# Kernel optimization log

Measured on AMD Instinct MI355X. Metric: run time of the kernel, lower is better.

The kernel has to match this reference:

```python
import jax, jax.numpy as jnp
import numpy as np

B, N, C = 4, 4096, 16
HID, OUT = 64, 64
ALL_K, K = 128, 32          # k + k_pos = 32
KD, KDP = 8, 6              # k_dilated, k_dilated_pos
EPS = 1e-5
NEG_SLOPE = 0.2


def setup_inputs() -> dict:
    ks = jax.random.split(jax.random.key(0), 12)
    C2, C4 = 2 * C, 4 * C
    return {
        "x": jax.random.normal(ks[0], (B, N, C), jnp.float32),
        "pos": jax.random.normal(ks[1], (B, N, 3), jnp.float32),
        "W1": jax.random.normal(ks[2], (C2, C2), jnp.float32) * 0.1,
        "g1": jnp.ones((C2,), jnp.float32),
        "b1": jnp.zeros((C2,), jnp.float32),
        "W2": jax.random.normal(ks[3], (HID, C4), jnp.float32) * 0.05,
        "g2": jnp.ones((HID,), jnp.float32),
        "b2": jnp.zeros((HID,), jnp.float32),
        "W3": jax.random.normal(ks[4], (OUT, HID), jnp.float32) * 0.05,
        "g3": jnp.ones((OUT,), jnp.float32),
        "b3": jnp.zeros((OUT,), jnp.float32),
    }


def pdist2(a):
    # squared pairwise distances (same top-k ordering as cdist p=2, and
    # avoids sqrt(0) on the diagonal). a: (B,N,D) -> (B,N,N)
    sq = jnp.sum(a * a, axis=-1)
    d = sq[:, :, None] + sq[:, None, :] - 2.0 * jnp.einsum('bnd,bmd->bnm', a, a)
    return jnp.maximum(d, 0.0)


def knn_excl_self(d2, k):
    # k nearest excluding self (self is the unique 0-distance nearest point)
    idx = jax.lax.top_k(-d2, k + 1)[1]
    return idx[..., 1:]


def fps(pts, npoint):
    # pts: (M, Kn, 3). Deterministic start at index 0 (torch version uses a
    # random start; only the sampled index set differs, math is identical).
    M, Kn, _ = pts.shape
    rows = jnp.arange(M)

    def body(i, state):
        centroids, distance, farthest = state
        centroids = centroids.at[:, i].set(farthest)
        centroid = pts[rows, farthest][:, None, :]            # (M,1,3)
        dist = jnp.sum((pts - centroid) ** 2, axis=-1)         # (M,Kn)
        distance = jnp.minimum(distance, dist)
        farthest = jnp.argmax(distance, axis=-1).astype(jnp.int32)
        return centroids, distance, farthest

    init = (jnp.zeros((M, npoint), jnp.int32),
            jnp.full((M, Kn), 1e10, jnp.float32),
            jnp.zeros((M,), jnp.int32))
    centroids, _, _ = jax.lax.fori_loop(0, npoint, body, init)
    return centroids


def edge_feat(feat, idx):
    # feat: (B,N,D) node features, idx: (B,N,Kn) neighbor indices
    # returns cat(neighbor - center, center): (B,N,Kn,2D)  (edge_function 249)
    nbr = feat[jnp.arange(feat.shape[0])[:, None, None], idx]  # (B,N,Kn,D)
    ctr = feat[:, :, None, :]
    return jnp.concatenate([nbr - ctr, jnp.broadcast_to(ctr, nbr.shape)], axis=-1)


def bn_lrelu(h, g, b):
    # BatchNorm2d with track_running_stats=False -> always batch stats.
    # h: (B,N,Kn,Cc), stats over (B,N,Kn) per channel.
    mu = jnp.mean(h, axis=(0, 1, 2), keepdims=True)
    var = jnp.var(h, axis=(0, 1, 2), keepdims=True)
    h = (h - mu) * jax.lax.rsqrt(var + EPS) * g + b
    return jnp.where(h > 0, h, NEG_SLOPE * h)


def reference(x, pos, W1, g1, b1, W2, g2, b2, W3, g3, b3):
    # --- dilated neighborhood: all_k nearest by position, FPS down to k ---
    cd2 = pdist2(pos)                                   # (B,N,N)
    idx_l = jax.lax.top_k(-cd2, ALL_K)[1]               # (B,N,ALL_K) incl. self
    idx_l_flat = idx_l.reshape(B * N, ALL_K)
    pts = pos.reshape(B * N, 3)[idx_l_flat]             # (B*N, ALL_K, 3)
    idx_fps_local = fps(pts, K)                         # (B*N, K)
    idx_fps = jnp.take_along_axis(idx_l_flat, idx_fps_local, axis=1)
    idx_fps = idx_fps.reshape(B, N, K)                  # (B,N,K)

    # --- dual kNN graph: k_dilated by feature distance + k_dilated_pos by pos ---
    idx_feat = knn_excl_self(pdist2(x), KD)             # (B,N,KD)
    idx_pos = knn_excl_self(cd2, KDP)                   # (B,N,KDP)
    idx1 = jnp.concatenate([idx_feat, idx_pos], axis=2)  # (B,N,KD+KDP)

    # --- conv1x1-BN-LeakyReLU on dual-graph edge features, max over nbrs ---
    e1 = edge_feat(x, idx1)                             # (B,N,14,2C)
    h1 = bn_lrelu(jnp.einsum('bnkc,oc->bnko', e1, W1), g1, b1)
    f1 = jnp.max(h1, axis=2)                            # (B,N,2C)

    # --- edge features on FPS-dilated graph, two conv1x1-BN-LeakyReLU ---
    e2 = edge_feat(f1, idx_fps)                         # (B,N,K,4C)
    h2 = bn_lrelu(jnp.einsum('bnkc,hc->bnkh', e2, W2), g2, b2)
    h3 = bn_lrelu(jnp.einsum('bnkh,oh->bnko', h2, W3), g3, b3)
    out = jnp.max(h3, axis=2)                           # (B,N,OUT)
    return out, idx1
```

## Files before the change

kernel.cpp:

```cpp
#include <hip/hip_runtime.h>

#define NPTS 4096
#define BNROWS 16384

__device__ __forceinline__ float lrelu(float h) { return h > 0.f ? h : 0.2f * h; }

#define WSYNC asm volatile("s_waitcnt lgkmcnt(0)" ::: "memory")

__global__ __launch_bounds__(512) void knn_pos_kernel(
    const float* __restrict__ pos, int* __restrict__ idx_l,
    int* __restrict__ idx1_i, float* __restrict__ idx1_f)
{
  __shared__ unsigned long long cKey[8][512];
  __shared__ unsigned int cCnt[8];
  int tid = threadIdx.x;
  int w = tid >> 6, lane = tid & 63;
  int r = blockIdx.x * 8 + w;
  int b = r >> 12, n = r & 4095;
  const float* pb = pos + (size_t)b * NPTS * 3;
  float cx = pb[n*3+0], cy = pb[n*3+1], cz = pb[n*3+2];
  if (lane == 0) cCnt[w] = 0u;
  WSYNC;

  unsigned int qp[32];
  int m1 = 65536, m2 = 65536, m3 = 65536;
  #pragma unroll
  for (int t = 0; t < 32; ++t) {
    unsigned int wq = 0u;
    #pragma unroll
    for (int h = 0; h < 2; ++h) {
      int j = (2*t + h) * 64 + lane;
      float dx = cx - pb[j*3+0], dy = cy - pb[j*3+1], dz = cz - pb[j*3+2];
      float d2 = dx*dx + dy*dy + dz*dz;
      int q = (int)(d2 * 1000.0f);
      q = q < 0 ? 0 : (q > 65535 ? 65535 : q);
      wq |= ((unsigned int)q) << (16*h);
      int nm1 = min(m1, q);
      int nm2 = min(m2, max(m1, q));
      int nm3 = min(m3, max(m2, q));
      m1 = nm1; m2 = nm2; m3 = nm3;
    }
    qp[t] = wq;
  }
  int lo = 0, hi = 65535;
  #pragma unroll
  for (int it = 0; it < 16; ++it) {
    int mid = (lo + hi) >> 1;
    int cnt = __popcll(__ballot(m3 <= mid));
    if (cnt >= 43) hi = mid; else lo = mid + 1;
  }
  unsigned int qt = (unsigned int)lo + 2u;

  #pragma unroll
  for (int t = 0; t < 32; ++t) {
    unsigned int wq = qp[t];
    unsigned int q0 = wq & 0xffffu, q1 = wq >> 16;
    if (q0 <= qt) { unsigned int p = atomicAdd(&cCnt[w], 1u); if (p < 512u) cKey[w][p] = (unsigned long long)((2*t)*64 + lane); }
    if (q1 <= qt) { unsigned int p = atomicAdd(&cCnt[w], 1u); if (p < 512u) cKey[w][p] = (unsigned long long)((2*t+1)*64 + lane); }
  }
  WSYNC;
  unsigned int nc = cCnt[w]; if (nc > 512u) nc = 512u;
  int M = (nc <= 256u) ? 256 : 512;
  int EPL = M >> 6;

  double cxd = (double)cx, cyd = (double)cy, czd = (double)cz;
  for (int t = 0; t < EPL; ++t) {
    int c = lane + (t << 6);
    unsigned long long kk = ~0ull;
    if (c < (int)nc) {
      int id = (int)cKey[w][c];
      double dx = cxd - (double)pb[id*3+0];
      double dy = cyd - (double)pb[id*3+1];
      double dz = czd - (double)pb[id*3+2];
      double d2 = dx*dx + dy*dy + dz*dz;
      unsigned long long bits = (unsigned long long)__double_as_longlong(d2);
      kk = (bits & ~0xFFFull) | (unsigned long long)(unsigned int)id;
    }
    cKey[w][c] = kk;
  }
  WSYNC;

  for (int k = 2; k <= M; k <<= 1) {
    for (int j = k >> 1; j > 0; j >>= 1) {
      for (int t = 0; t < EPL; ++t) {
        int i = lane + (t << 6);
        int ixj = i ^ j;
        if (ixj > i) {
          unsigned long long ka = cKey[w][i], kb = cKey[w][ixj];
          bool up = ((i & k) == 0);
          if ((ka > kb) == up) { cKey[w][i] = kb; cKey[w][ixj] = ka; }
        }
      }
      WSYNC;
    }
  }
  idx_l[(size_t)r * 128 + lane]      = (int)(cKey[w][lane] & 0xFFFull);
  idx_l[(size_t)r * 128 + lane + 64] = (int)(cKey[w][lane + 64] & 0xFFFull);
  if (lane < 6) {
    int v = (int)(cKey[w][1 + lane] & 0xFFFull);
    idx1_i[r * 14 + 8 + lane] = v;
    idx1_f[r * 14 + 8 + lane] = (float)v;
  }
}

__global__ __launch_bounds__(512) void knn_feat_kernel(
    const float* __restrict__ x, int* __restrict__ idx1_i, float* __restrict__ idx1_f)
{
  __shared__ float ctrf[8][16];
  __shared__ float4 cm2[8][5];
  __shared__ unsigned short lmin[8][512];
  __shared__ int cand[8][192];
  __shared__ unsigned int cCnt[8];
  __shared__ unsigned short qtS[8];
  int tid = threadIdx.x;
  int rbase = blockIdx.x * 8;
  int b = rbase >> 12;
  const float* xb = x + (size_t)b * NPTS * 16;

  if (tid < 128) {
    int rr = tid >> 4, c = tid & 15;
    float v = xb[(size_t)((rbase + rr) & 4095) * 16 + c];
    ctrf[rr][c] = v;
    ((float*)&cm2[rr][0])[c] = -2.0f * v;
  }
  if (tid < 8) cCnt[tid] = 0u;
  __syncthreads();
  if (tid < 8) {
    float s = 0.f;
    for (int c = 0; c < 16; ++c) { float v = ctrf[tid][c]; s += v * v; }
    cm2[tid][4].x = s;
  }
  __syncthreads();

  unsigned int qp[8][4];
  int minq[8];
  #pragma unroll
  for (int r = 0; r < 8; ++r) minq[r] = 65536;

  #pragma unroll
  for (int pp = 0; pp < 4; ++pp) {
    int j0 = tid + 512 * (2*pp);
    int j1 = j0 + 512;
    const float4* xj0 = (const float4*)(xb + (size_t)j0 * 16);
    const float4* xj1 = (const float4*)(xb + (size_t)j1 * 16);
    float4 a0 = xj0[0], a1 = xj0[1], a2 = xj0[2], a3 = xj0[3];
    float4 b0 = xj1[0], b1 = xj1[1], b2 = xj1[2], b3 = xj1[3];
    float va[16] = {a0.x,a0.y,a0.z,a0.w, a1.x,a1.y,a1.z,a1.w,
                    a2.x,a2.y,a2.z,a2.w, a3.x,a3.y,a3.z,a3.w};
    float vb[16] = {b0.x,b0.y,b0.z,b0.w, b1.x,b1.y,b1.z,b1.w,
                    b2.x,b2.y,b2.z,b2.w, b3.x,b3.y,b3.z,b3.w};
    float pna = 0.f, pnb = 0.f;
    #pragma unroll
    for (int c = 0; c < 16; ++c) { pna = fmaf(va[c], va[c], pna); pnb = fmaf(vb[c], vb[c], pnb); }
    #pragma unroll
    for (int r = 0; r < 8; ++r) {
      float4 m0 = cm2[r][0], m1 = cm2[r][1], m2 = cm2[r][2], m3 = cm2[r][3];
      float c2 = cm2[r][4].x;
      float wm[16] = {m0.x,m0.y,m0.z,m0.w, m1.x,m1.y,m1.z,m1.w,
                      m2.x,m2.y,m2.z,m2.w, m3.x,m3.y,m3.z,m3.w};
      float aa = pna + c2, ab = pnb + c2;
      #pragma unroll
      for (int c = 0; c < 16; ++c) { aa = fmaf(wm[c], va[c], aa); ab = fmaf(wm[c], vb[c], ab); }
      int qa = (int)(aa * 400.0f); qa = qa < 0 ? 0 : (qa > 65535 ? 65535 : qa);
      int qb = (int)(ab * 400.0f); qb = qb < 0 ? 0 : (qb > 65535 ? 65535 : qb);
      qp[r][pp] = (unsigned int)qa | ((unsigned int)qb << 16);
      minq[r] = min(minq[r], min(qa, qb));
    }
  }
  #pragma unroll
  for (int r = 0; r < 8; ++r) lmin[r][tid] = (unsigned short)minq[r];
  __syncthreads();

  int w = tid >> 6, lane = tid & 63;
  {
    unsigned short lv[8];
    #pragma unroll
    for (int t = 0; t < 8; ++t) lv[t] = lmin[w][lane + 64*t];
    int lo = 0, hi = 65535;
    #pragma unroll
    for (int it = 0; it < 16; ++it) {
      int mid = (lo + hi) >> 1;
      int cnt = 0;
      #pragma unroll
      for (int t = 0; t < 8; ++t) cnt += __popcll(__ballot((int)lv[t] <= mid));
      if (cnt >= 10) hi = mid; else lo = mid + 1;
    }
    if (lane == 0) qtS[w] = (unsigned short)min(lo + 2, 65535);
  }
  __syncthreads();

  {
    unsigned int qts[8];
    #pragma unroll
    for (int r = 0; r < 8; ++r) qts[r] = qtS[r];
    #pragma unroll
    for (int r = 0; r < 8; ++r) {
      #pragma unroll
      for (int pp = 0; pp < 4; ++pp) {
        unsigned int wq = qp[r][pp];
        unsigned int q0 = wq & 0xffffu, q1 = wq >> 16;
        if (q0 <= qts[r]) { unsigned int p = atomicAdd(&cCnt[r], 1u); if (p < 192u) cand[r][p] = tid + 512*(2*pp); }
        if (q1 <= qts[r]) { unsigned int p = atomicAdd(&cCnt[r], 1u); if (p < 192u) cand[r][p] = tid + 512*(2*pp+1); }
      }
    }
  }
  __syncthreads();

  {
    int nc = (int)cCnt[w]; if (nc > 192) nc = 192;
    double key[3]; int kid[3];
    #pragma unroll
    for (int s = 0; s < 3; ++s) {
      int c = lane + 64*s;
      if (c < nc) {
        int id = cand[w][c];
        const float4* xp = (const float4*)(xb + (size_t)id * 16);
        float4 q0 = xp[0], q1 = xp[1], q2 = xp[2], q3 = xp[3];
        float xv[16] = {q0.x,q0.y,q0.z,q0.w, q1.x,q1.y,q1.z,q1.w,
                        q2.x,q2.y,q2.z,q2.w, q3.x,q3.y,q3.z,q3.w};
        double acc = 0.0;
        #pragma unroll
        for (int c2 = 0; c2 < 16; ++c2) { double d = (double)ctrf[w][c2] - (double)xv[c2]; acc += d * d; }
        key[s] = acc; kid[s] = id;
      } else { key[s] = 1e300; kid[s] = 0x7fffffff; }
    }
    int row = rbase + w;
    for (int it = 0; it < 9; ++it) {
      double bk = key[0]; int bi = kid[0], bs = 0;
      if (key[1] < bk || (key[1] == bk && kid[1] < bi)) { bk = key[1]; bi = kid[1]; bs = 1; }
      if (key[2] < bk || (key[2] == bk && kid[2] < bi)) { bk = key[2]; bi = kid[2]; bs = 2; }
      double rk = bk; int ri = bi;
      #pragma unroll
      for (int off = 32; off > 0; off >>= 1) {
        double ok = __shfl_xor(rk, off, 64);
        int oi = __shfl_xor(ri, off, 64);
        if (ok < rk || (ok == rk && oi < ri)) { rk = ok; ri = oi; }
      }
      if (it > 0 && lane == 0) {
        idx1_i[row * 14 + it - 1] = ri;
        idx1_f[row * 14 + it - 1] = (float)ri;
      }
      if (bi == ri) key[bs] = 1e300;
    }
  }
}

__global__ __launch_bounds__(256) void fps_kernel(
    const float* __restrict__ pos, const int* __restrict__ idx_l, int* __restrict__ idx_fps)
{
  int wave = threadIdx.x >> 6, lane = threadIdx.x & 63;
  int r = blockIdx.x * 4 + wave;
  const int* il = idx_l + (size_t)r * 128;
  int gi0 = il[lane], gi1 = il[lane + 64];
  double x0 = (double)pos[gi0*3+0], y0 = (double)pos[gi0*3+1], z0 = (double)pos[gi0*3+2];
  double x1 = (double)pos[gi1*3+0], y1 = (double)pos[gi1*3+1], z1 = (double)pos[gi1*3+2];
  double d0 = 1e10, d1 = 1e10;
  int far = 0;
  int* outp = idx_fps + (size_t)r * 32;
  for (int i = 0; i < 32; ++i) {
    int ownerLane = far & 63;
    int sel = far >> 6;
    int gsel = sel ? gi1 : gi0;
    int gout = __shfl(gsel, ownerLane, 64);
    if (lane == 0) outp[i] = gout;
    double cx = __shfl(sel ? x1 : x0, ownerLane, 64);
    double cy = __shfl(sel ? y1 : y0, ownerLane, 64);
    double cz = __shfl(sel ? z1 : z0, ownerLane, 64);
    double t0 = (x0-cx)*(x0-cx) + (y0-cy)*(y0-cy) + (z0-cz)*(z0-cz);
    double t1 = (x1-cx)*(x1-cx) + (y1-cy)*(y1-cy) + (z1-cz)*(z1-cz);
    d0 = fmin(d0, t0); d1 = fmin(d1, t1);
    double v; int p;
    if (d1 > d0) { v = d1; p = lane + 64; } else { v = d0; p = lane; }
    for (int off = 32; off > 0; off >>= 1) {
      double ov = __shfl_xor(v, off, 64);
      int op = __shfl_xor(p, off, 64);
      if (ov > v || (ov == v && op < p)) { v = ov; p = op; }
    }
    far = p;
  }
}

__global__ __launch_bounds__(256) void sv_kernel(
    const float* __restrict__ x, const float* __restrict__ W1,
    float* __restrict__ s, float* __restrict__ v)
{
  __shared__ float xs[8][16];
  __shared__ float w1t[512], w1dt[512];
  int tid = threadIdx.x;
  int rbase = blockIdx.x * 8;
  for (int i = tid; i < 512; i += 256) {
    int c = i >> 5, o = i & 31;
    float a = W1[o * 32 + c], bb = W1[o * 32 + 16 + c];
    w1t[i] = a; w1dt[i] = bb - a;
  }
  if (tid < 128) { int rr = tid >> 4, c = tid & 15; xs[rr][c] = x[(size_t)(rbase + rr) * 16 + c]; }
  __syncthreads();
  int rr = tid >> 5, o = tid & 31;
  float sa = 0.f, va = 0.f;
  #pragma unroll
  for (int c = 0; c < 16; ++c) {
    float xv = xs[rr][c];
    sa = fmaf(xv, w1t[c * 32 + o], sa);
    va = fmaf(xv, w1dt[c * 32 + o], va);
  }
  int r = rbase + rr;
  s[(size_t)r * 32 + o] = sa;
  v[(size_t)r * 32 + o] = va;
}

__global__ __launch_bounds__(256) void h1stats_kernel(
    const float* __restrict__ s, const float* __restrict__ v, const int* __restrict__ idx1_i,
    double* __restrict__ slotsH1, float* __restrict__ h1max)
{
  __shared__ int sidx[8][14];
  __shared__ float sred[256], sred2[256];
  int tid = threadIdx.x;
  int rr = tid >> 5, o = tid & 31;
  int rbase = blockIdx.x * 8;
  if (tid < 112) { int q = tid / 14, k = tid % 14; sidx[q][k] = idx1_i[(rbase + q) * 14 + k]; }
  __syncthreads();
  int r = rbase + rr;
  int broff = r & ~4095;
  float vv = v[(size_t)r * 32 + o];
  float m = -3.4e38f, ls = 0.f, lss = 0.f;
  #pragma unroll
  for (int k = 0; k < 14; ++k) {
    int j = sidx[rr][k];
    float val = s[(size_t)(broff + j) * 32 + o] + vv;
    m = fmaxf(m, val);
    ls += val; lss += val * val;
  }
  h1max[(size_t)r * 32 + o] = m;
  sred[tid] = ls; sred2[tid] = lss;
  __syncthreads();
  if (tid < 32) {
    float s2 = 0.f, ss = 0.f;
    #pragma unroll
    for (int j = 0; j < 8; ++j) { s2 += sred[j * 32 + tid]; ss += sred2[j * 32 + tid]; }
    int slot = blockIdx.x & 255;
    atomicAdd(&slotsH1[slot * 64 + tid], (double)s2);
    atomicAdd(&slotsH1[slot * 64 + 32 + tid], (double)ss);
  }
}

__global__ void finalize_stats_kernel(const double* __restrict__ slots, int C, double cnt,
    const float* __restrict__ g, const float* __restrict__ bta, float* __restrict__ scsh)
{
  int o = threadIdx.x;
  if (o < C) {
    double s = 0.0, ss = 0.0;
    for (int slot = 0; slot < 256; ++slot) { s += slots[slot * 2 * C + o]; ss += slots[slot * 2 * C + C + o]; }
    double mu = s / cnt;
    double var = ss / cnt - mu * mu;
    double rs = 1.0 / sqrt(var + 1e-5);
    float sc = (float)rs * g[o];
    float sh = bta[o] - (float)mu * sc;
    scsh[o] = sc;
    scsh[C + o] = sh;
  }
}

__global__ __launch_bounds__(256) void tu_kernel(
    const float* __restrict__ h1max, const float* __restrict__ scsh1, const float* __restrict__ W2,
    float* __restrict__ t, float* __restrict__ u)
{
  __shared__ float f1s[4][32];
  __shared__ float w2t[2048], w2dt[2048];
  int tid = threadIdx.x;
  int rbase = blockIdx.x * 4;
  for (int i = tid; i < 2048; i += 256) {
    int c = i >> 6, o = i & 63;
    float a = W2[o * 64 + c], bb = W2[o * 64 + 32 + c];
    w2t[i] = a; w2dt[i] = bb - a;
  }
  if (tid < 128) {
    int rr = tid >> 5, c = tid & 31;
    f1s[rr][c] = lrelu(h1max[(size_t)(rbase + rr) * 32 + c] * scsh1[c] + scsh1[32 + c]);
  }
  __syncthreads();
  int rr = tid >> 6, o = tid & 63;
  float ta = 0.f, ua = 0.f;
  #pragma unroll
  for (int c = 0; c < 32; ++c) {
    float fv = f1s[rr][c];
    ta = fmaf(fv, w2t[c * 64 + o], ta);
    ua = fmaf(fv, w2dt[c * 64 + o], ua);
  }
  int r = rbase + rr;
  t[(size_t)r * 64 + o] = ta;
  u[(size_t)r * 64 + o] = ua;
}

__global__ __launch_bounds__(256) void h2stats_kernel(
    const float* __restrict__ t, const float* __restrict__ u, const int* __restrict__ idx_fps,
    double* __restrict__ slotsH2)
{
  __shared__ int nids[8][32];
  __shared__ float sred[256], sred2[256];
  int tid = threadIdx.x;
  int o = tid & 63, wv = tid >> 6;
  int rbase = blockIdx.x * 8;
  { int q = tid >> 5, k = tid & 31; nids[q][k] = idx_fps[(rbase + q) * 32 + k]; }
  __syncthreads();
  float ls = 0.f, lss = 0.f;
  for (int rr = 0; rr < 8; ++rr) {
    int r = rbase + rr;
    int broff = r & ~4095;
    float uo = u[(size_t)r * 64 + o];
    #pragma unroll
    for (int i = 0; i < 8; ++i) {
      int k = wv + 4 * i;
      float val = t[(size_t)(broff + nids[rr][k]) * 64 + o] + uo;
      ls += val; lss += val * val;
    }
  }
  sred[tid] = ls; sred2[tid] = lss;
  __syncthreads();
  if (tid < 64) {
    float s2 = sred[tid] + sred[tid + 64] + sred[tid + 128] + sred[tid + 192];
    float ss = sred2[tid] + sred2[tid + 64] + sred2[tid + 128] + sred2[tid + 192];
    int slot = blockIdx.x & 255;
    atomicAdd(&slotsH2[slot * 128 + tid], (double)s2);
    atomicAdd(&slotsH2[slot * 128 + 64 + tid], (double)ss);
  }
}

#define ROWS3 8
__global__ __launch_bounds__(256, 4) void h3_kernel(
    const float* __restrict__ t, const float* __restrict__ u, const int* __restrict__ idx_fps,
    const float* __restrict__ W3, const float* __restrict__ scsh2,
    double* __restrict__ slotsH3, float* __restrict__ h3max)
{
  __shared__ float h2lds[2048];
  __shared__ float wmax[256];
  __shared__ float sred[256], sred2[256];
  __shared__ int nids[ROWS3][32];
  int tid = threadIdx.x;
  int o = tid & 63, wv = tid >> 6;
  float4 w3r[16];
  const float4* w3p = (const float4*)(W3 + o * 64);
  #pragma unroll
  for (int j = 0; j < 16; ++j) w3r[j] = w3p[j];
  float sc2o = scsh2[o], sh2o = scsh2[64 + o];
  int rbase = blockIdx.x * ROWS3;
  { int q = tid >> 5, k = tid & 31; nids[q][k] = idx_fps[(rbase + q) * 32 + k]; }
  float ls = 0.f, lss = 0.f;
  __syncthreads();
  for (int rr = 0; rr < ROWS3; ++rr) {
    int r = rbase + rr;
    int broff = r & ~4095;
    float uo = u[(size_t)r * 64 + o];
    #pragma unroll
    for (int i = 0; i < 8; ++i) {
      int k = wv + 4 * i;
      float val = t[(size_t)(broff + nids[rr][k]) * 64 + o] + uo;
      h2lds[k * 64 + o] = lrelu(val * sc2o + sh2o);
    }
    __syncthreads();
    float kmax = -3.4e38f;
    #pragma unroll
    for (int i = 0; i < 8; ++i) {
      int k = wv + 4 * i;
      const float4* hp = (const float4*)(h2lds + k * 64);
      float acc = 0.f;
      #pragma unroll
      for (int j = 0; j < 16; ++j) {
        float4 h = hp[j];
        acc = fmaf(h.x, w3r[j].x, acc); acc = fmaf(h.y, w3r[j].y, acc);
        acc = fmaf(h.z, w3r[j].z, acc); acc = fmaf(h.w, w3r[j].w, acc);
      }
      ls += acc; lss += acc * acc;
      kmax = fmaxf(kmax, acc);
    }
    wmax[tid] = kmax;
    __syncthreads();
    if (tid < 64) {
      float m = fmaxf(fmaxf(wmax[tid], wmax[64 + tid]), fmaxf(wmax[128 + tid], wmax[192 + tid]));
      h3max[(size_t)r * 64 + tid] = m;
    }
  }
  sred[tid] = ls; sred2[tid] = lss;
  __syncthreads();
  if (tid < 64) {
    float s2 = sred[tid] + sred[tid + 64] + sred[tid + 128] + sred[tid + 192];
    float ss = sred2[tid] + sred2[tid + 64] + sred2[tid + 128] + sred2[tid + 192];
    int slot = blockIdx.x & 255;
    atomicAdd(&slotsH3[slot * 128 + tid], (double)s2);
    atomicAdd(&slotsH3[slot * 128 + 64 + tid], (double)ss);
  }
}

__global__ void out_kernel(const float* __restrict__ h3max, const float* __restrict__ scsh3,
                           float* __restrict__ out)
{
  int i = blockIdx.x * 256 + threadIdx.x;
  int o = i & 63;
  out[i] = lrelu(h3max[i] * scsh3[o] + scsh3[64 + o]);
}

extern "C" void kernel_launch(void* const* d_in, const int* in_sizes, int n_in,
                              void* d_out, int out_size, void* d_ws, size_t ws_size,
                              hipStream_t stream) {
  (void)in_sizes; (void)n_in; (void)out_size; (void)ws_size;
  const float* x   = (const float*)d_in[0];
  const float* pos = (const float*)d_in[1];
  const float* W1  = (const float*)d_in[2];
  const float* g1  = (const float*)d_in[3];
  const float* b1  = (const float*)d_in[4];
  const float* W2  = (const float*)d_in[5];
  const float* g2  = (const float*)d_in[6];
  const float* b2  = (const float*)d_in[7];
  const float* W3  = (const float*)d_in[8];
  const float* g3  = (const float*)d_in[9];
  const float* b3  = (const float*)d_in[10];

  float* out      = (float*)d_out;
  float* out_idx1 = out + 1048576;

  char* ws = (char*)d_ws;
  double* slotsH1 = (double*)(ws + 0);
  double* slotsH2 = (double*)(ws + 131072);
  double* slotsH3 = (double*)(ws + 393216);
  float*  scsh1   = (float*)(ws + 655360);
  float*  scsh2   = (float*)(ws + 655616);
  float*  scsh3   = (float*)(ws + 656128);
  int*    idx_l   = (int*)(ws + 1048576);
  float*  t_buf   = (float*)(ws + 1048576);
  float*  u_buf   = (float*)(ws + 5242880);
  int*    idx_fps = (int*)(ws + 9437184);
  int*    idx1_i  = (int*)(ws + 11534336);
  float*  h1max   = (float*)(ws + 12451840);
  float*  s_buf   = (float*)(ws + 14548992);
  float*  v_buf   = (float*)(ws + 16646144);
  float*  h3max   = (float*)(ws + 18743296);

  hipMemsetAsync(d_ws, 0, 656640, stream);

  knn_pos_kernel <<<dim3(2048), dim3(512), 0, stream>>>(pos, idx_l, idx1_i, out_idx1);
  knn_feat_kernel<<<dim3(2048), dim3(512), 0, stream>>>(x, idx1_i, out_idx1);
  fps_kernel     <<<dim3(4096), dim3(256), 0, stream>>>(pos, idx_l, idx_fps);
  sv_kernel      <<<dim3(2048), dim3(256), 0, stream>>>(x, W1, s_buf, v_buf);
  h1stats_kernel <<<dim3(2048), dim3(256), 0, stream>>>(s_buf, v_buf, idx1_i, slotsH1, h1max);
  finalize_stats_kernel<<<dim3(1), dim3(64), 0, stream>>>(slotsH1, 32, 229376.0, g1, b1, scsh1);
  tu_kernel      <<<dim3(4096), dim3(256), 0, stream>>>(h1max, scsh1, W2, t_buf, u_buf);
  h2stats_kernel <<<dim3(2048), dim3(256), 0, stream>>>(t_buf, u_buf, idx_fps, slotsH2);
  finalize_stats_kernel<<<dim3(1), dim3(64), 0, stream>>>(slotsH2, 64, 524288.0, g2, b2, scsh2);
  h3_kernel      <<<dim3(2048), dim3(256), 0, stream>>>(t_buf, u_buf, idx_fps, W3, scsh2, slotsH3, h3max);
  finalize_stats_kernel<<<dim3(1), dim3(64), 0, stream>>>(slotsH3, 64, 524288.0, g3, b3, scsh3);
  out_kernel     <<<dim3(4096), dim3(256), 0, stream>>>(h3max, scsh3, out);
}
```

Baseline: 654.3 us.

## Restructure feature kNN: precomputed norms, 4 rows per block, float keys

Adds a small kernel that precomputes squared norms of the feature rows. The feature kNN kernel now handles 4 query rows per 256-thread block instead of 8 per 512. Query weights sit in uniform registers via readfirstlane, and full float distance keys replace the 16-bit quantised ones. The threshold search runs a 31-step bisection over float bit patterns, with a small slack before candidate collection. This removes the per-point norm recomputation and quantisation work and should raise occupancy. The costs are more reloads of the x data across blocks, 64 float keys held in registers per thread, and a longer bisection.

```diff
diff --git a/kernel.cpp b/kernel.cpp
--- a/kernel.cpp
+++ b/kernel.cpp
@@ -6,6 +6,23 @@
 __device__ __forceinline__ float lrelu(float h) { return h > 0.f ? h : 0.2f * h; }
 
 #define WSYNC asm volatile("s_waitcnt lgkmcnt(0)" ::: "memory")
+
+__device__ __forceinline__ float rfl(float v) {
+  return __int_as_float(__builtin_amdgcn_readfirstlane(__float_as_int(v)));
+}
+
+__global__ __launch_bounds__(256) void norms_kernel(
+    const float* __restrict__ x, float* __restrict__ sqx)
+{
+  int r = blockIdx.x * 256 + threadIdx.x;
+  const float4* xp = (const float4*)(x + (size_t)r * 16);
+  float4 a0 = xp[0], a1 = xp[1], a2 = xp[2], a3 = xp[3];
+  float s = a0.x*a0.x + a0.y*a0.y + a0.z*a0.z + a0.w*a0.w
+          + a1.x*a1.x + a1.y*a1.y + a1.z*a1.z + a1.w*a1.w
+          + a2.x*a2.x + a2.y*a2.y + a2.z*a2.z + a2.w*a2.w
+          + a3.x*a3.x + a3.y*a3.y + a3.z*a3.z + a3.w*a3.w;
+  sqx[r] = s;
+}
 
 __global__ __launch_bounds__(512) void knn_pos_kernel(
     const float* __restrict__ pos, int* __restrict__ idx_l,
@@ -103,112 +120,96 @@
   }
 }
 
-__global__ __launch_bounds__(512) void knn_feat_kernel(
-    const float* __restrict__ x, int* __restrict__ idx1_i, float* __restrict__ idx1_f)
-{
-  __shared__ float ctrf[8][16];
-  __shared__ float4 cm2[8][5];
-  __shared__ unsigned short lmin[8][512];
-  __shared__ int cand[8][192];
-  __shared__ unsigned int cCnt[8];
-  __shared__ unsigned short qtS[8];
-  int tid = threadIdx.x;
-  int rbase = blockIdx.x * 8;
+__global__ __launch_bounds__(256) void knn_feat_kernel(
+    const float* __restrict__ x, const float* __restrict__ sqx,
+    int* __restrict__ idx1_i, float* __restrict__ idx1_f)
+{
+  __shared__ float lmin[4][256];
+  __shared__ int cand[4][192];
+  __shared__ unsigned int cCnt[4];
+  __shared__ float qtS[4];
+  __shared__ float ctrf[4][16];
+  int tid = threadIdx.x;
+  int w = tid >> 6, lane = tid & 63;
+  int rbase = blockIdx.x * 4;
   int b = rbase >> 12;
   const float* xb = x + (size_t)b * NPTS * 16;
-
-  if (tid < 128) {
+  const float* sqb = sqx + b * NPTS;
+
+  if (tid < 64) {
     int rr = tid >> 4, c = tid & 15;
-    float v = xb[(size_t)((rbase + rr) & 4095) * 16 + c];
-    ctrf[rr][c] = v;
-    ((float*)&cm2[rr][0])[c] = -2.0f * v;
-  }
-  if (tid < 8) cCnt[tid] = 0u;
-  __syncthreads();
-  if (tid < 8) {
+    ctrf[rr][c] = xb[(size_t)((rbase + rr) & 4095) * 16 + c];
+  }
+  if (tid < 4) cCnt[tid] = 0u;
+  __syncthreads();
+
+  float cm[4][16], c2[4];
+  #pragma unroll
+  for (int rr = 0; rr < 4; ++rr) {
     float s = 0.f;
-    for (int c = 0; c < 16; ++c) { float v = ctrf[tid][c]; s += v * v; }
-    cm2[tid][4].x = s;
-  }
-  __syncthreads();
-
-  unsigned int qp[8][4];
-  int minq[8];
-  #pragma unroll
-  for (int r = 0; r < 8; ++r) minq[r] = 65536;
-
-  #pragma unroll
-  for (int pp = 0; pp < 4; ++pp) {
-    int j0 = tid + 512 * (2*pp);
-    int j1 = j0 + 512;
-    const float4* xj0 = (const float4*)(xb + (size_t)j0 * 16);
-    const float4* xj1 = (const float4*)(xb + (size_t)j1 * 16);
-    float4 a0 = xj0[0], a1 = xj0[1], a2 = xj0[2], a3 = xj0[3];
-    float4 b0 = xj1[0], b1 = xj1[1], b2 = xj1[2], b3 = xj1[3];
+    #pragma unroll
+    for (int c = 0; c < 16; ++c) {
+      float v = ctrf[rr][c];
+      cm[rr][c] = rfl(-2.0f * v);
+      s = fmaf(v, v, s);
+    }
+    c2[rr] = rfl(s);
+  }
+
+  float key[4][16];
+  float fk[4] = {3.4e38f, 3.4e38f, 3.4e38f, 3.4e38f};
+  #pragma unroll
+  for (int pt = 0; pt < 16; ++pt) {
+    int j = tid + 256 * pt;
+    const float4* xj = (const float4*)(xb + (size_t)j * 16);
+    float4 a0 = xj[0], a1 = xj[1], a2 = xj[2], a3 = xj[3];
+    float sqj = sqb[j];
     float va[16] = {a0.x,a0.y,a0.z,a0.w, a1.x,a1.y,a1.z,a1.w,
                     a2.x,a2.y,a2.z,a2.w, a3.x,a3.y,a3.z,a3.w};
-    float vb[16] = {b0.x,b0.y,b0.z,b0.w, b1.x,b1.y,b1.z,b1.w,
-                    b2.x,b2.y,b2.z,b2.w, b3.x,b3.y,b3.z,b3.w};
-    float pna = 0.f, pnb = 0.f;
-    #pragma unroll
-    for (int c = 0; c < 16; ++c) { pna = fmaf(va[c], va[c], pna); pnb = fmaf(vb[c], vb[c], pnb); }
-    #pragma unroll
-    for (int r = 0; r < 8; ++r) {
-      float4 m0 = cm2[r][0], m1 = cm2[r][1], m2 = cm2[r][2], m3 = cm2[r][3];
-      float c2 = cm2[r][4].x;
-      float wm[16] = {m0.x,m0.y,m0.z,m0.w, m1.x,m1.y,m1.z,m1.w,
-                      m2.x,m2.y,m2.z,m2.w, m3.x,m3.y,m3.z,m3.w};
-      float aa = pna + c2, ab = pnb + c2;
+    #pragma unroll
+    for (int rr = 0; rr < 4; ++rr) {
+      float acc = sqj + c2[rr];
       #pragma unroll
-      for (int c = 0; c < 16; ++c) { aa = fmaf(wm[c], va[c], aa); ab = fmaf(wm[c], vb[c], ab); }
-      int qa = (int)(aa * 400.0f); qa = qa < 0 ? 0 : (qa > 65535 ? 65535 : qa);
-      int qb = (int)(ab * 400.0f); qb = qb < 0 ? 0 : (qb > 65535 ? 65535 : qb);
-      qp[r][pp] = (unsigned int)qa | ((unsigned int)qb << 16);
-      minq[r] = min(minq[r], min(qa, qb));
-    }
-  }
-  #pragma unroll
-  for (int r = 0; r < 8; ++r) lmin[r][tid] = (unsigned short)minq[r];
-  __syncthreads();
-
-  int w = tid >> 6, lane = tid & 63;
+      for (int c = 0; c < 16; ++c) acc = fmaf(va[c], cm[rr][c], acc);
+      key[rr][pt] = acc;
+      fk[rr] = fminf(fk[rr], acc);
+    }
+  }
+  #pragma unroll
+  for (int rr = 0; rr < 4; ++rr) lmin[rr][tid] = fk[rr];
+  __syncthreads();
+
   {
-    unsigned short lv[8];
-    #pragma unroll
-    for (int t = 0; t < 8; ++t) lv[t] = lmin[w][lane + 64*t];
-    int lo = 0, hi = 65535;
-    #pragma unroll
-    for (int it = 0; it < 16; ++it) {
-      int mid = (lo + hi) >> 1;
-      int cnt = 0;
-      #pragma unroll
-      for (int t = 0; t < 8; ++t) cnt += __popcll(__ballot((int)lv[t] <= mid));
+    float lv0 = lmin[w][lane], lv1 = lmin[w][lane + 64];
+    float lv2 = lmin[w][lane + 128], lv3 = lmin[w][lane + 192];
+    unsigned int lo = 0u, hi = 0x7F800000u;
+    for (int it = 0; it < 31; ++it) {
+      unsigned int mid = (lo + hi) >> 1;
+      float midf = __uint_as_float(mid);
+      int cnt = __popcll(__ballot(lv0 <= midf)) + __popcll(__ballot(lv1 <= midf))
+              + __popcll(__ballot(lv2 <= midf)) + __popcll(__ballot(lv3 <= midf));
       if (cnt >= 10) hi = mid; else lo = mid + 1;
     }
-    if (lane == 0) qtS[w] = (unsigned short)min(lo + 2, 65535);
+    if (lane == 0) qtS[w] = __uint_as_float(hi) * 1.0002f + 1e-3f;
   }
   __syncthreads();
 
   {
-    unsigned int qts[8];
-    #pragma unroll
-    for (int r = 0; r < 8; ++r) qts[r] = qtS[r];
-    #pragma unroll
-    for (int r = 0; r < 8; ++r) {
-      #pragma unroll
-      for (int pp = 0; pp < 4; ++pp) {
-        unsigned int wq = qp[r][pp];
-        unsigned int q0 = wq & 0xffffu, q1 = wq >> 16;
-        if (q0 <= qts[r]) { unsigned int p = atomicAdd(&cCnt[r], 1u); if (p < 192u) cand[r][p] = tid + 512*(2*pp); }
-        if (q1 <= qts[r]) { unsigned int p = atomicAdd(&cCnt[r], 1u); if (p < 192u) cand[r][p] = tid + 512*(2*pp+1); }
-      }
+    float q0 = qtS[0], q1 = qtS[1], q2 = qtS[2], q3 = qtS[3];
+    #pragma unroll
+    for (int pt = 0; pt < 16; ++pt) {
+      int j = tid + 256 * pt;
+      if (key[0][pt] <= q0) { unsigned int p = atomicAdd(&cCnt[0], 1u); if (p < 192u) cand[0][p] = j; }
+      if (key[1][pt] <= q1) { unsigned int p = atomicAdd(&cCnt[1], 1u); if (p < 192u) cand[1][p] = j; }
+      if (key[2][pt] <= q2) { unsigned int p = atomicAdd(&cCnt[2], 1u); if (p < 192u) cand[2][p] = j; }
+      if (key[3][pt] <= q3) { unsigned int p = atomicAdd(&cCnt[3], 1u); if (p < 192u) cand[3][p] = j; }
     }
   }
   __syncthreads();
 
   {
     int nc = (int)cCnt[w]; if (nc > 192) nc = 192;
-    double key[3]; int kid[3];
+    double key64[3]; int kid[3];
     #pragma unroll
     for (int s = 0; s < 3; ++s) {
       int c = lane + 64*s;
@@ -220,15 +221,15 @@
                         q2.x,q2.y,q2.z,q2.w, q3.x,q3.y,q3.z,q3.w};
         double acc = 0.0;
         #pragma unroll
-        for (int c2 = 0; c2 < 16; ++c2) { double d = (double)ctrf[w][c2] - (double)xv[c2]; acc += d * d; }
-        key[s] = acc; kid[s] = id;
-      } else { key[s] = 1e300; kid[s] = 0x7fffffff; }
+        for (int c2i = 0; c2i < 16; ++c2i) { double d = (double)ctrf[w][c2i] - (double)xv[c2i]; acc += d * d; }
+        key64[s] = acc; kid[s] = id;
+      } else { key64[s] = 1e300; kid[s] = 0x7fffffff; }
     }
     int row = rbase + w;
     for (int it = 0; it < 9; ++it) {
-      double bk = key[0]; int bi = kid[0], bs = 0;
-      if (key[1] < bk || (key[1] == bk && kid[1] < bi)) { bk = key[1]; bi = kid[1]; bs = 1; }
-      if (key[2] < bk || (key[2] == bk && kid[2] < bi)) { bk = key[2]; bi = kid[2]; bs = 2; }
+      double bk = key64[0]; int bi = kid[0], bs = 0;
+      if (key64[1] < bk || (key64[1] == bk && kid[1] < bi)) { bk = key64[1]; bi = kid[1]; bs = 1; }
+      if (key64[2] < bk || (key64[2] == bk && kid[2] < bi)) { bk = key64[2]; bi = kid[2]; bs = 2; }
       double rk = bk; int ri = bi;
       #pragma unroll
       for (int off = 32; off > 0; off >>= 1) {
@@ -240,7 +241,7 @@
         idx1_i[row * 14 + it - 1] = ri;
         idx1_f[row * 14 + it - 1] = (float)ri;
       }
-      if (bi == ri) key[bs] = 1e300;
+      if (bi == ri) key64[bs] = 1e300;
     }
   }
 }
@@ -524,6 +525,7 @@
   float*  scsh1   = (float*)(ws + 655360);
   float*  scsh2   = (float*)(ws + 655616);
   float*  scsh3   = (float*)(ws + 656128);
+  float*  sqx     = (float*)(ws + 786432);
   int*    idx_l   = (int*)(ws + 1048576);
   float*  t_buf   = (float*)(ws + 1048576);
   float*  u_buf   = (float*)(ws + 5242880);
@@ -536,8 +538,9 @@
 
   hipMemsetAsync(d_ws, 0, 656640, stream);
 
+  norms_kernel   <<<dim3(64),   dim3(256), 0, stream>>>(x, sqx);
   knn_pos_kernel <<<dim3(2048), dim3(512), 0, stream>>>(pos, idx_l, idx1_i, out_idx1);
-  knn_feat_kernel<<<dim3(2048), dim3(512), 0, stream>>>(x, idx1_i, out_idx1);
+  knn_feat_kernel<<<dim3(4096), dim3(256), 0, stream>>>(x, sqx, idx1_i, out_idx1);
   fps_kernel     <<<dim3(4096), dim3(256), 0, stream>>>(pos, idx_l, idx_fps);
   sv_kernel      <<<dim3(2048), dim3(256), 0, stream>>>(x, W1, s_buf, v_buf);
   h1stats_kernel <<<dim3(2048), dim3(256), 0, stream>>>(s_buf, v_buf, idx1_i, slotsH1, h1max);
```

Result: slower. 667.9 us (+2.1%).
